# Optimization experiments

Hardware: AMD Instinct MI355X
Metric: run time of the kernel (lower is better)

Reference implementation:

```python
import jax, jax.numpy as jnp
import numpy as np

B, S, D, H = 2, 1024, 1024, 16
DH = D // H
EPS = 1e-5

def _ln(x, g, b):
    m = jnp.mean(x, axis=-1, keepdims=True)
    v = jnp.mean((x - m) ** 2, axis=-1, keepdims=True)
    return (x - m) / jnp.sqrt(v + EPS) * g + b

def setup_inputs() -> dict:
    key = jax.random.key(0)
    ks = jax.random.split(key, 5)
    scale = 1.0 / np.sqrt(D)
    return {
        "id": jax.random.normal(ks[0], (B, S, D), dtype=jnp.float32),
        "Wq": jax.random.uniform(ks[1], (D, D), jnp.float32, -scale, scale),
        "Wk": jax.random.uniform(ks[2], (D, D), jnp.float32, -scale, scale),
        "Wv": jax.random.uniform(ks[3], (D, D), jnp.float32, -scale, scale),
        "g0": jnp.ones((D,), jnp.float32), "b0": jnp.zeros((D,), jnp.float32),
        "g1": jnp.ones((D,), jnp.float32), "b1": jnp.zeros((D,), jnp.float32),
        "g2": jnp.ones((D,), jnp.float32), "b2": jnp.zeros((D,), jnp.float32),
    }

def reference(id, Wq, Wk, Wv, g0, b0, g1, b1, g2, b2):
    residual = id
    id_ln = _ln(id, g0, b0)
    # torch Linear: x @ W.T ; split heads along last dim, cat along batch
    q = (id_ln @ Wq.T).reshape(B, S, H, DH)
    k = (id_ln @ Wk.T).reshape(B, S, H, DH)
    v = (id_ln @ Wv.T).reshape(B, S, H, DH)
    scores = jnp.einsum('bqhd,bkhd->bhqk', q, k) / np.sqrt(DH)
    A = jax.nn.softmax(scores, axis=-1)                      # [B,H,S,S]
    O = jnp.einsum('bhqk,bkhd->bqhd', A, v).reshape(B, S, D)  # merge heads
    left = _ln(id_ln + O, g1, b1)
    right = _ln(residual + O, g2, b2)
    out = left + right
    # torch layout of A is [(H*B), S, S] with head-major ordering
    A_out = jnp.transpose(A, (1, 0, 2, 3)).reshape(H * B, S, S)
    return (out, A_out)
```

## Files before the change

kernel.cpp:

```cpp
#include <hip/hip_runtime.h>

namespace {

constexpr int B = 2, S = 1024, D = 1024, H = 16, DH = 64;
constexpr int M = B * S;
constexpr float EPS = 1e-5f;

using bf16x8 = __attribute__((ext_vector_type(8))) short;
using f32x4  = __attribute__((ext_vector_type(4))) float;

typedef const __attribute__((address_space(1))) void* gptr_t;
typedef __attribute__((address_space(3))) void* lptr_t;

__device__ __forceinline__ unsigned short f2bf(float f) {
    union { float f; unsigned u; } v{f};
    unsigned r = v.u + 0x7fffu + ((v.u >> 16) & 1u);
    return (unsigned short)(r >> 16);
}

__device__ __forceinline__ float wave_sum(float v) {
#pragma unroll
    for (int off = 32; off > 0; off >>= 1) v += __shfl_down(v, off, 64);
    return v;
}

__global__ __launch_bounds__(256) void cvt_w_kernel(
    const float* __restrict__ Wq, const float* __restrict__ Wk,
    const float* __restrict__ Wv, unsigned short* __restrict__ Wb)
{
    const float* src = (blockIdx.z == 0) ? Wq : (blockIdx.z == 1) ? Wk : Wv;
    const size_t i = ((size_t)blockIdx.x * 256 + threadIdx.x) * 4;
    float4 f = *reinterpret_cast<const float4*>(src + i);
    ushort4 h;
    h.x = f2bf(f.x); h.y = f2bf(f.y); h.z = f2bf(f.z); h.w = f2bf(f.w);
    *reinterpret_cast<ushort4*>(Wb + (size_t)blockIdx.z * D * D + i) = h;
}

__global__ __launch_bounds__(256) void ln0_kernel(
    const float* __restrict__ x, const float* __restrict__ g,
    const float* __restrict__ bt, float* __restrict__ y,
    unsigned short* __restrict__ yb)
{
    __shared__ float sm[8];
    __shared__ float stats[2];
    const int row = blockIdx.x;
    const int t = threadIdx.x;
    const float4 v = reinterpret_cast<const float4*>(x + (size_t)row * D)[t];
    float s  = v.x + v.y + v.z + v.w;
    float ss = v.x*v.x + v.y*v.y + v.z*v.z + v.w*v.w;
    s = wave_sum(s); ss = wave_sum(ss);
    const int lane = t & 63, wid = t >> 6;
    if (lane == 0) { sm[wid] = s; sm[4 + wid] = ss; }
    __syncthreads();
    if (t == 0) {
        float S1 = sm[0] + sm[1] + sm[2] + sm[3];
        float S2 = sm[4] + sm[5] + sm[6] + sm[7];
        float m  = S1 * (1.0f / D);
        float var = S2 * (1.0f / D) - m * m;
        stats[0] = m; stats[1] = rsqrtf(var + EPS);
    }
    __syncthreads();
    const float m = stats[0], r = stats[1];
    const float4 gv = reinterpret_cast<const float4*>(g)[t];
    const float4 bv = reinterpret_cast<const float4*>(bt)[t];
    float4 o;
    o.x = (v.x - m) * r * gv.x + bv.x;
    o.y = (v.y - m) * r * gv.y + bv.y;
    o.z = (v.z - m) * r * gv.z + bv.z;
    o.w = (v.w - m) * r * gv.w + bv.w;
    reinterpret_cast<float4*>(y + (size_t)row * D)[t] = o;
    ushort4 h; h.x = f2bf(o.x); h.y = f2bf(o.y); h.z = f2bf(o.z); h.w = f2bf(o.w);
    *reinterpret_cast<ushort4*>(yb + (size_t)row * D + t * 4) = h;
}

__global__ __launch_bounds__(256) void qkv_mfma_kernel(
    const unsigned short* __restrict__ idln, const unsigned short* __restrict__ Wb,
    unsigned short* __restrict__ q, unsigned short* __restrict__ k,
    unsigned short* __restrict__ vT)
{
    __shared__ unsigned short As[128 * 32];
    __shared__ unsigned short Bs[128 * 32];
    const int zi = blockIdx.z;
    const unsigned short* Bmat = Wb + (size_t)zi * D * D;
    const int m0 = blockIdx.y * 128, n0 = blockIdx.x * 128;
    const int t = threadIdx.x;
    const int w = t >> 6, lane = t & 63;
    const int wm = (w >> 1) * 64, wn = (w & 1) * 64;
    const int quad = lane >> 4, l16 = lane & 15;
    const int srow = t >> 2;
    const int scol = (t & 3) * 8;

    f32x4 acc[4][4];
#pragma unroll
    for (int i = 0; i < 4; ++i)
#pragma unroll
        for (int j = 0; j < 4; ++j) acc[i][j] = (f32x4){0.f, 0.f, 0.f, 0.f};

    for (int k0 = 0; k0 < D; k0 += 32) {
        __syncthreads();
#pragma unroll
        for (int c = 0; c < 2; ++c) {
            const unsigned short* ga = idln + (size_t)(m0 + srow + c * 64) * D + k0 + scol;
            __builtin_amdgcn_global_load_lds((gptr_t)ga, (lptr_t)(As + t * 8 + c * 2048), 16, 0, 0);
            const unsigned short* gb = Bmat + (size_t)(n0 + srow + c * 64) * D + k0 + scol;
            __builtin_amdgcn_global_load_lds((gptr_t)gb, (lptr_t)(Bs + t * 8 + c * 2048), 16, 0, 0);
        }
        __syncthreads();
        bf16x8 af[4], bfr[4];
#pragma unroll
        for (int i = 0; i < 4; ++i)
            af[i] = *reinterpret_cast<const bf16x8*>(As + (wm + i * 16 + l16) * 32 + quad * 8);
#pragma unroll
        for (int j = 0; j < 4; ++j)
            bfr[j] = *reinterpret_cast<const bf16x8*>(Bs + (wn + j * 16 + l16) * 32 + quad * 8);
#pragma unroll
        for (int i = 0; i < 4; ++i)
#pragma unroll
            for (int j = 0; j < 4; ++j)
                acc[i][j] = __builtin_amdgcn_mfma_f32_16x16x32_bf16(af[i], bfr[j], acc[i][j], 0, 0, 0);
    }

    if (zi < 2) {
        unsigned short* C = (zi == 0) ? q : k;
#pragma unroll
        for (int i = 0; i < 4; ++i)
#pragma unroll
            for (int j = 0; j < 4; ++j) {
                const int gcol = n0 + wn + j * 16 + l16;
#pragma unroll
                for (int reg = 0; reg < 4; ++reg) {
                    const int grow = m0 + wm + i * 16 + quad * 4 + reg;
                    C[(size_t)grow * D + gcol] = f2bf(acc[i][j][reg]);
                }
            }
    } else {
        const int b = m0 >> 10;
#pragma unroll
        for (int i = 0; i < 4; ++i)
#pragma unroll
            for (int j = 0; j < 4; ++j) {
                const int gcol = n0 + wn + j * 16 + l16;
                const int srow0 = (m0 - b * S) + wm + i * 16 + quad * 4;
                ushort4 h;
                h.x = f2bf(acc[i][j][0]); h.y = f2bf(acc[i][j][1]);
                h.z = f2bf(acc[i][j][2]); h.w = f2bf(acc[i][j][3]);
                *reinterpret_cast<ushort4*>(vT + ((size_t)b * D + gcol) * S + srow0) = h;
            }
    }
}

__global__ __launch_bounds__(256) void scores_mfma_kernel(
    const unsigned short* __restrict__ q, const unsigned short* __restrict__ k,
    float* __restrict__ Eout, float* __restrict__ rowsum)
{
    __shared__ unsigned short As[128 * 32];
    __shared__ unsigned short Bs[128 * 32];
    const int z = blockIdx.z;
    const int b = z & 1, h = z >> 1;
    const int m0 = blockIdx.y * 128, n0 = blockIdx.x * 128;
    const int t = threadIdx.x;
    const int w = t >> 6, lane = t & 63;
    const int wm = (w >> 1) * 64, wn = (w & 1) * 64;
    const int quad = lane >> 4, l16 = lane & 15;
    const int srow = t >> 2;
    const int scol = (t & 3) * 8;

    f32x4 acc[4][4];
#pragma unroll
    for (int i = 0; i < 4; ++i)
#pragma unroll
        for (int j = 0; j < 4; ++j) acc[i][j] = (f32x4){0.f, 0.f, 0.f, 0.f};

    for (int k0 = 0; k0 < DH; k0 += 32) {
        __syncthreads();
#pragma unroll
        for (int c = 0; c < 2; ++c) {
            const unsigned short* ga = q + (size_t)(b * S + m0 + srow + c * 64) * D + h * DH + k0 + scol;
            __builtin_amdgcn_global_load_lds((gptr_t)ga, (lptr_t)(As + t * 8 + c * 2048), 16, 0, 0);
            const unsigned short* gb = k + (size_t)(b * S + n0 + srow + c * 64) * D + h * DH + k0 + scol;
            __builtin_amdgcn_global_load_lds((gptr_t)gb, (lptr_t)(Bs + t * 8 + c * 2048), 16, 0, 0);
        }
        __syncthreads();
        bf16x8 af[4], bfr[4];
#pragma unroll
        for (int i = 0; i < 4; ++i)
            af[i] = *reinterpret_cast<const bf16x8*>(As + (wm + i * 16 + l16) * 32 + quad * 8);
#pragma unroll
        for (int j = 0; j < 4; ++j)
            bfr[j] = *reinterpret_cast<const bf16x8*>(Bs + (wn + j * 16 + l16) * 32 + quad * 8);
#pragma unroll
        for (int i = 0; i < 4; ++i)
#pragma unroll
            for (int j = 0; j < 4; ++j)
                acc[i][j] = __builtin_amdgcn_mfma_f32_16x16x32_bf16(af[i], bfr[j], acc[i][j], 0, 0, 0);
    }

    float* Ez = Eout + (size_t)z * S * S;
    float part[4][4];
#pragma unroll
    for (int i = 0; i < 4; ++i)
#pragma unroll
        for (int reg = 0; reg < 4; ++reg) part[i][reg] = 0.f;

#pragma unroll
    for (int i = 0; i < 4; ++i)
#pragma unroll
        for (int j = 0; j < 4; ++j) {
            const int gcol = n0 + wn + j * 16 + l16;
#pragma unroll
            for (int reg = 0; reg < 4; ++reg) {
                const int grow = m0 + wm + i * 16 + quad * 4 + reg;
                float e = __expf(acc[i][j][reg] * 0.125f);
                Ez[(size_t)grow * S + gcol] = e;
                part[i][reg] += e;
            }
        }
#pragma unroll
    for (int i = 0; i < 4; ++i)
#pragma unroll
        for (int reg = 0; reg < 4; ++reg) {
            float p = part[i][reg];
#pragma unroll
            for (int off = 1; off < 16; off <<= 1) p += __shfl_xor(p, off, 64);
            part[i][reg] = p;
        }
    if (l16 == 0) {
#pragma unroll
        for (int i = 0; i < 4; ++i)
#pragma unroll
            for (int reg = 0; reg < 4; ++reg) {
                const int grow = m0 + wm + i * 16 + quad * 4 + reg;
                atomicAdd(&rowsum[(size_t)z * S + grow], part[i][reg]);
            }
    }
}

__global__ __launch_bounds__(256) void ov_mfma_kernel(
    float* __restrict__ Eio, const unsigned short* __restrict__ vT,
    const float* __restrict__ rowsum, float* __restrict__ O)
{
    __shared__ unsigned short Es[128 * 32];
    __shared__ unsigned short Vs[64 * 32];
    __shared__ float sInv[128];
    const int z = blockIdx.z;
    const int b = z & 1, h = z >> 1;
    const int m0 = blockIdx.y * 128;
    const int t = threadIdx.x;
    const int w = t >> 6, lane = t & 63;
    const int wm = w * 32;
    const int quad = lane >> 4, l16 = lane & 15;

    if (t < 128) sInv[t] = 1.0f / rowsum[(size_t)z * S + m0 + t];

    float* Ez = Eio + (size_t)z * S * S;

    f32x4 acc[2][4];
#pragma unroll
    for (int i = 0; i < 2; ++i)
#pragma unroll
        for (int j = 0; j < 4; ++j) acc[i][j] = (f32x4){0.f, 0.f, 0.f, 0.f};

    const int er = t >> 1;
    const int ec = (t & 1) * 16;

    for (int k0 = 0; k0 < S; k0 += 32) {
        __syncthreads();
        {
            const unsigned short* gv = vT + ((size_t)b * D + h * DH + (t >> 2)) * S + k0 + (t & 3) * 8;
            __builtin_amdgcn_global_load_lds((gptr_t)gv, (lptr_t)(Vs + t * 8), 16, 0, 0);
        }
        {
            float* gE = Ez + (size_t)(m0 + er) * S + k0 + ec;
            const float inv = sInv[er];
#pragma unroll
            for (int u = 0; u < 4; ++u) {
                float4 f = *reinterpret_cast<const float4*>(gE + u * 4);
                float4 fn = make_float4(f.x * inv, f.y * inv, f.z * inv, f.w * inv);
                *reinterpret_cast<float4*>(gE + u * 4) = fn;
                ushort4 hh;
                hh.x = f2bf(f.x); hh.y = f2bf(f.y); hh.z = f2bf(f.z); hh.w = f2bf(f.w);
                *reinterpret_cast<ushort4*>(Es + er * 32 + ec + u * 4) = hh;
            }
        }
        __syncthreads();
        bf16x8 af[2], bfr[4];
#pragma unroll
        for (int i = 0; i < 2; ++i)
            af[i] = *reinterpret_cast<const bf16x8*>(Es + (wm + i * 16 + l16) * 32 + quad * 8);
#pragma unroll
        for (int j = 0; j < 4; ++j)
            bfr[j] = *reinterpret_cast<const bf16x8*>(Vs + (j * 16 + l16) * 32 + quad * 8);
#pragma unroll
        for (int i = 0; i < 2; ++i)
#pragma unroll
            for (int j = 0; j < 4; ++j)
                acc[i][j] = __builtin_amdgcn_mfma_f32_16x16x32_bf16(af[i], bfr[j], acc[i][j], 0, 0, 0);
    }

#pragma unroll
    for (int i = 0; i < 2; ++i)
#pragma unroll
        for (int j = 0; j < 4; ++j) {
            const int gcol = h * DH + j * 16 + l16;
#pragma unroll
            for (int reg = 0; reg < 4; ++reg) {
                const int lrow = wm + i * 16 + quad * 4 + reg;
                O[(size_t)(b * S + m0 + lrow) * D + gcol] = acc[i][j][reg] * sInv[lrow];
            }
        }
}

__global__ __launch_bounds__(256) void final_kernel(
    const float* __restrict__ id, const float* __restrict__ id_ln, const float* __restrict__ O,
    const float* __restrict__ g1, const float* __restrict__ b1,
    const float* __restrict__ g2, const float* __restrict__ b2,
    float* __restrict__ out)
{
    __shared__ float sm[16];
    __shared__ float stats[4];
    const int row = blockIdx.x;
    const int t = threadIdx.x;
    const size_t base = (size_t)row * D;
    const float4 xi = reinterpret_cast<const float4*>(id + base)[t];
    const float4 xl = reinterpret_cast<const float4*>(id_ln + base)[t];
    const float4 xo = reinterpret_cast<const float4*>(O + base)[t];
    float4 t1, t2;
    t1.x = xl.x + xo.x; t1.y = xl.y + xo.y; t1.z = xl.z + xo.z; t1.w = xl.w + xo.w;
    t2.x = xi.x + xo.x; t2.y = xi.y + xo.y; t2.z = xi.z + xo.z; t2.w = xi.w + xo.w;
    float s1  = t1.x + t1.y + t1.z + t1.w;
    float ss1 = t1.x*t1.x + t1.y*t1.y + t1.z*t1.z + t1.w*t1.w;
    float s2  = t2.x + t2.y + t2.z + t2.w;
    float ss2 = t2.x*t2.x + t2.y*t2.y + t2.z*t2.z + t2.w*t2.w;
    s1 = wave_sum(s1); ss1 = wave_sum(ss1);
    s2 = wave_sum(s2); ss2 = wave_sum(ss2);
    const int lane = t & 63, wid = t >> 6;
    if (lane == 0) { sm[wid] = s1; sm[4+wid] = ss1; sm[8+wid] = s2; sm[12+wid] = ss2; }
    __syncthreads();
    if (t == 0) {
        float S1 = sm[0]+sm[1]+sm[2]+sm[3];
        float Q1 = sm[4]+sm[5]+sm[6]+sm[7];
        float S2 = sm[8]+sm[9]+sm[10]+sm[11];
        float Q2 = sm[12]+sm[13]+sm[14]+sm[15];
        float m1 = S1 * (1.0f / D);
        float m2 = S2 * (1.0f / D);
        stats[0] = m1; stats[1] = rsqrtf(Q1 * (1.0f / D) - m1*m1 + EPS);
        stats[2] = m2; stats[3] = rsqrtf(Q2 * (1.0f / D) - m2*m2 + EPS);
    }
    __syncthreads();
    const float m1 = stats[0], r1 = stats[1], m2 = stats[2], r2 = stats[3];
    const float4 g1v = reinterpret_cast<const float4*>(g1)[t];
    const float4 b1v = reinterpret_cast<const float4*>(b1)[t];
    const float4 g2v = reinterpret_cast<const float4*>(g2)[t];
    const float4 b2v = reinterpret_cast<const float4*>(b2)[t];
    float4 o;
    o.x = (t1.x - m1)*r1*g1v.x + b1v.x + (t2.x - m2)*r2*g2v.x + b2v.x;
    o.y = (t1.y - m1)*r1*g1v.y + b1v.y + (t2.y - m2)*r2*g2v.y + b2v.y;
    o.z = (t1.z - m1)*r1*g1v.z + b1v.z + (t2.z - m2)*r2*g2v.z + b2v.z;
    o.w = (t1.w - m1)*r1*g1v.w + b1v.w + (t2.w - m2)*r2*g2v.w + b2v.w;
    reinterpret_cast<float4*>(out + base)[t] = o;
}

}

extern "C" void kernel_launch(void* const* d_in, const int* in_sizes, int n_in,
                              void* d_out, int out_size, void* d_ws, size_t ws_size,
                              hipStream_t stream)
{
    const float* id = (const float*)d_in[0];
    const float* Wq = (const float*)d_in[1];
    const float* Wk = (const float*)d_in[2];
    const float* Wv = (const float*)d_in[3];
    const float* g0 = (const float*)d_in[4];
    const float* b0 = (const float*)d_in[5];
    const float* g1 = (const float*)d_in[6];
    const float* b1 = (const float*)d_in[7];
    const float* g2 = (const float*)d_in[8];
    const float* b2 = (const float*)d_in[9];

    float* out  = (float*)d_out;
    float* Eout = out + (size_t)B * S * D;

    char* ws = (char*)d_ws;
    float* id_ln  = (float*)(ws);
    float* O      = (float*)(ws + (8u << 20));
    float* rowsum = (float*)(ws + (16u << 20));
    unsigned short* idln_bf = (unsigned short*)(ws + (16u << 20) + (128u << 10));
    unsigned short* Wb      = idln_bf + (size_t)M * D;
    unsigned short* qb      = Wb + (size_t)3 * D * D;
    unsigned short* kb      = qb + (size_t)M * D;
    unsigned short* vT      = kb + (size_t)M * D;

    hipMemsetAsync(rowsum, 0, (size_t)H * B * S * sizeof(float), stream);
    hipLaunchKernelGGL(cvt_w_kernel, dim3(D * D / 1024, 1, 3), dim3(256), 0, stream,
                       Wq, Wk, Wv, Wb);
    hipLaunchKernelGGL(ln0_kernel, dim3(M), dim3(256), 0, stream, id, g0, b0, id_ln, idln_bf);
    hipLaunchKernelGGL(qkv_mfma_kernel, dim3(D / 128, M / 128, 3), dim3(256), 0, stream,
                       idln_bf, Wb, qb, kb, vT);
    hipLaunchKernelGGL(scores_mfma_kernel, dim3(S / 128, S / 128, H * B), dim3(256), 0, stream,
                       qb, kb, Eout, rowsum);
    hipLaunchKernelGGL(ov_mfma_kernel, dim3(1, S / 128, H * B), dim3(256), 0, stream,
                       Eout, vT, rowsum, O);
    hipLaunchKernelGGL(final_kernel, dim3(M), dim3(256), 0, stream,
                       id, id_ln, O, g1, b1, g2, b2, out);
}
```

Baseline: 276.1 us.

## Fuse scores and PV into one two-pass attention kernel

Replaces the separate scores kernel (writing unnormalized exp to A, plus atomic row sums) and the PV kernel (re-reading A, normalizing, writing back) with one kernel per 64-row query tile. The first pass computes QK^T only to accumulate row sums. The second pass recomputes QK^T, writes normalized A once, and feeds bf16 probabilities from LDS into the PV MFMA. This removes a full read and rewrite of the 128 MB attention matrix, the memset and the atomics. The cost is doubled QK^T compute and more LDS per block.

After: 233.3 us. -15.5%, faster.

```diff
diff --git a/kernel.cpp b/kernel.cpp
--- a/kernel.cpp
+++ b/kernel.cpp
@@ -149,164 +149,157 @@
     }
 }
 
-__global__ __launch_bounds__(256) void scores_mfma_kernel(
+__global__ __launch_bounds__(256) void attn_fused_kernel(
     const unsigned short* __restrict__ q, const unsigned short* __restrict__ k,
-    float* __restrict__ Eout, float* __restrict__ rowsum)
-{
-    __shared__ unsigned short As[128 * 32];
-    __shared__ unsigned short Bs[128 * 32];
+    const unsigned short* __restrict__ vT, float* __restrict__ Aout,
+    float* __restrict__ O)
+{
+    __shared__ unsigned short Qs[2 * 64 * 32];
+    __shared__ unsigned short Ks[2 * 128 * 32];
+    __shared__ unsigned short Vs[4 * 64 * 32];
+    __shared__ unsigned short Ps[4 * 64 * 32];
+    __shared__ float rs[4][64];
+    __shared__ float sInv[64];
+
     const int z = blockIdx.z;
     const int b = z & 1, h = z >> 1;
-    const int m0 = blockIdx.y * 128, n0 = blockIdx.x * 128;
+    const int m0 = blockIdx.y * 64;
     const int t = threadIdx.x;
     const int w = t >> 6, lane = t & 63;
-    const int wm = (w >> 1) * 64, wn = (w & 1) * 64;
     const int quad = lane >> 4, l16 = lane & 15;
-    const int srow = t >> 2;
-    const int scol = (t & 3) * 8;
-
-    f32x4 acc[4][4];
+    const int wn = w * 32;
+    const int sr = t >> 2, sc8 = (t & 3) * 8;
+
+#pragma unroll
+    for (int c = 0; c < 2; ++c) {
+        const unsigned short* gq = q + (size_t)(b * S + m0 + sr) * D + h * DH + c * 32 + sc8;
+        __builtin_amdgcn_global_load_lds((gptr_t)gq, (lptr_t)(Qs + c * 2048 + t * 8), 16, 0, 0);
+    }
+
+    float part[4][4];
 #pragma unroll
     for (int i = 0; i < 4; ++i)
 #pragma unroll
-        for (int j = 0; j < 4; ++j) acc[i][j] = (f32x4){0.f, 0.f, 0.f, 0.f};
-
-    for (int k0 = 0; k0 < DH; k0 += 32) {
-        __syncthreads();
+        for (int r = 0; r < 4; ++r) part[i][r] = 0.f;
+
+    for (int n0 = 0; n0 < S; n0 += 128) {
+        __syncthreads();
+#pragma unroll
+        for (int c = 0; c < 2; ++c)
+#pragma unroll
+            for (int cc = 0; cc < 2; ++cc) {
+                const unsigned short* gk = k + (size_t)(b * S + n0 + cc * 64 + sr) * D + h * DH + c * 32 + sc8;
+                __builtin_amdgcn_global_load_lds((gptr_t)gk, (lptr_t)(Ks + c * 4096 + cc * 2048 + t * 8), 16, 0, 0);
+            }
+        __syncthreads();
+        f32x4 acc[4][2];
+#pragma unroll
+        for (int i = 0; i < 4; ++i)
+#pragma unroll
+            for (int j = 0; j < 2; ++j) acc[i][j] = (f32x4){0.f, 0.f, 0.f, 0.f};
 #pragma unroll
         for (int c = 0; c < 2; ++c) {
-            const unsigned short* ga = q + (size_t)(b * S + m0 + srow + c * 64) * D + h * DH + k0 + scol;
-            __builtin_amdgcn_global_load_lds((gptr_t)ga, (lptr_t)(As + t * 8 + c * 2048), 16, 0, 0);
-            const unsigned short* gb = k + (size_t)(b * S + n0 + srow + c * 64) * D + h * DH + k0 + scol;
-            __builtin_amdgcn_global_load_lds((gptr_t)gb, (lptr_t)(Bs + t * 8 + c * 2048), 16, 0, 0);
-        }
-        __syncthreads();
-        bf16x8 af[4], bfr[4];
-#pragma unroll
-        for (int i = 0; i < 4; ++i)
-            af[i] = *reinterpret_cast<const bf16x8*>(As + (wm + i * 16 + l16) * 32 + quad * 8);
-#pragma unroll
-        for (int j = 0; j < 4; ++j)
-            bfr[j] = *reinterpret_cast<const bf16x8*>(Bs + (wn + j * 16 + l16) * 32 + quad * 8);
-#pragma unroll
-        for (int i = 0; i < 4; ++i)
-#pragma unroll
-            for (int j = 0; j < 4; ++j)
-                acc[i][j] = __builtin_amdgcn_mfma_f32_16x16x32_bf16(af[i], bfr[j], acc[i][j], 0, 0, 0);
-    }
-
-    float* Ez = Eout + (size_t)z * S * S;
-    float part[4][4];
+            bf16x8 af[4], bfr[2];
+#pragma unroll
+            for (int i = 0; i < 4; ++i)
+                af[i] = *reinterpret_cast<const bf16x8*>(Qs + c * 2048 + (i * 16 + l16) * 32 + quad * 8);
+#pragma unroll
+            for (int j = 0; j < 2; ++j)
+                bfr[j] = *reinterpret_cast<const bf16x8*>(Ks + c * 4096 + (wn + j * 16 + l16) * 32 + quad * 8);
+#pragma unroll
+            for (int i = 0; i < 4; ++i)
+#pragma unroll
+                for (int j = 0; j < 2; ++j)
+                    acc[i][j] = __builtin_amdgcn_mfma_f32_16x16x32_bf16(af[i], bfr[j], acc[i][j], 0, 0, 0);
+        }
+#pragma unroll
+        for (int i = 0; i < 4; ++i)
+#pragma unroll
+            for (int j = 0; j < 2; ++j)
+#pragma unroll
+                for (int r = 0; r < 4; ++r)
+                    part[i][r] += __expf(acc[i][j][r] * 0.125f);
+    }
 #pragma unroll
     for (int i = 0; i < 4; ++i)
 #pragma unroll
-        for (int reg = 0; reg < 4; ++reg) part[i][reg] = 0.f;
-
-#pragma unroll
-    for (int i = 0; i < 4; ++i)
-#pragma unroll
-        for (int j = 0; j < 4; ++j) {
-            const int gcol = n0 + wn + j * 16 + l16;
-#pragma unroll
-            for (int reg = 0; reg < 4; ++reg) {
-                const int grow = m0 + wm + i * 16 + quad * 4 + reg;
-                float e = __expf(acc[i][j][reg] * 0.125f);
-                Ez[(size_t)grow * S + gcol] = e;
-                part[i][reg] += e;
-            }
-        }
-#pragma unroll
-    for (int i = 0; i < 4; ++i)
-#pragma unroll
-        for (int reg = 0; reg < 4; ++reg) {
-            float p = part[i][reg];
+        for (int r = 0; r < 4; ++r) {
+            float p = part[i][r];
 #pragma unroll
             for (int off = 1; off < 16; off <<= 1) p += __shfl_xor(p, off, 64);
-            part[i][reg] = p;
-        }
-    if (l16 == 0) {
-#pragma unroll
-        for (int i = 0; i < 4; ++i)
-#pragma unroll
-            for (int reg = 0; reg < 4; ++reg) {
-                const int grow = m0 + wm + i * 16 + quad * 4 + reg;
-                atomicAdd(&rowsum[(size_t)z * S + grow], part[i][reg]);
-            }
-    }
-}
-
-__global__ __launch_bounds__(256) void ov_mfma_kernel(
-    float* __restrict__ Eio, const unsigned short* __restrict__ vT,
-    const float* __restrict__ rowsum, float* __restrict__ O)
-{
-    __shared__ unsigned short Es[128 * 32];
-    __shared__ unsigned short Vs[64 * 32];
-    __shared__ float sInv[128];
-    const int z = blockIdx.z;
-    const int b = z & 1, h = z >> 1;
-    const int m0 = blockIdx.y * 128;
-    const int t = threadIdx.x;
-    const int w = t >> 6, lane = t & 63;
-    const int wm = w * 32;
-    const int quad = lane >> 4, l16 = lane & 15;
-
-    if (t < 128) sInv[t] = 1.0f / rowsum[(size_t)z * S + m0 + t];
-
-    float* Ez = Eio + (size_t)z * S * S;
-
-    f32x4 acc[2][4];
-#pragma unroll
-    for (int i = 0; i < 2; ++i)
-#pragma unroll
-        for (int j = 0; j < 4; ++j) acc[i][j] = (f32x4){0.f, 0.f, 0.f, 0.f};
-
-    const int er = t >> 1;
-    const int ec = (t & 1) * 16;
-
-    for (int k0 = 0; k0 < S; k0 += 32) {
-        __syncthreads();
-        {
-            const unsigned short* gv = vT + ((size_t)b * D + h * DH + (t >> 2)) * S + k0 + (t & 3) * 8;
-            __builtin_amdgcn_global_load_lds((gptr_t)gv, (lptr_t)(Vs + t * 8), 16, 0, 0);
-        }
-        {
-            float* gE = Ez + (size_t)(m0 + er) * S + k0 + ec;
-            const float inv = sInv[er];
-#pragma unroll
-            for (int u = 0; u < 4; ++u) {
-                float4 f = *reinterpret_cast<const float4*>(gE + u * 4);
-                float4 fn = make_float4(f.x * inv, f.y * inv, f.z * inv, f.w * inv);
-                *reinterpret_cast<float4*>(gE + u * 4) = fn;
-                ushort4 hh;
-                hh.x = f2bf(f.x); hh.y = f2bf(f.y); hh.z = f2bf(f.z); hh.w = f2bf(f.w);
-                *reinterpret_cast<ushort4*>(Es + er * 32 + ec + u * 4) = hh;
-            }
-        }
-        __syncthreads();
-        bf16x8 af[2], bfr[4];
-#pragma unroll
-        for (int i = 0; i < 2; ++i)
-            af[i] = *reinterpret_cast<const bf16x8*>(Es + (wm + i * 16 + l16) * 32 + quad * 8);
-#pragma unroll
-        for (int j = 0; j < 4; ++j)
-            bfr[j] = *reinterpret_cast<const bf16x8*>(Vs + (j * 16 + l16) * 32 + quad * 8);
-#pragma unroll
-        for (int i = 0; i < 2; ++i)
-#pragma unroll
-            for (int j = 0; j < 4; ++j)
-                acc[i][j] = __builtin_amdgcn_mfma_f32_16x16x32_bf16(af[i], bfr[j], acc[i][j], 0, 0, 0);
-    }
-
-#pragma unroll
-    for (int i = 0; i < 2; ++i)
-#pragma unroll
-        for (int j = 0; j < 4; ++j) {
-            const int gcol = h * DH + j * 16 + l16;
-#pragma unroll
-            for (int reg = 0; reg < 4; ++reg) {
-                const int lrow = wm + i * 16 + quad * 4 + reg;
-                O[(size_t)(b * S + m0 + lrow) * D + gcol] = acc[i][j][reg] * sInv[lrow];
-            }
+            if (l16 == 0) rs[w][i * 16 + quad * 4 + r] = p;
+        }
+    __syncthreads();
+    if (t < 64) sInv[t] = 1.0f / (rs[0][t] + rs[1][t] + rs[2][t] + rs[3][t]);
+
+    float* Az = Aout + (size_t)z * S * S;
+    f32x4 accO[4];
+#pragma unroll
+    for (int j = 0; j < 4; ++j) accO[j] = (f32x4){0.f, 0.f, 0.f, 0.f};
+
+    for (int n0 = 0; n0 < S; n0 += 128) {
+        __syncthreads();
+#pragma unroll
+        for (int c = 0; c < 2; ++c)
+#pragma unroll
+            for (int cc = 0; cc < 2; ++cc) {
+                const unsigned short* gk = k + (size_t)(b * S + n0 + cc * 64 + sr) * D + h * DH + c * 32 + sc8;
+                __builtin_amdgcn_global_load_lds((gptr_t)gk, (lptr_t)(Ks + c * 4096 + cc * 2048 + t * 8), 16, 0, 0);
+            }
+#pragma unroll
+        for (int ks = 0; ks < 4; ++ks) {
+            const unsigned short* gv = vT + ((size_t)b * D + h * DH + sr) * S + n0 + ks * 32 + sc8;
+            __builtin_amdgcn_global_load_lds((gptr_t)gv, (lptr_t)(Vs + ks * 2048 + t * 8), 16, 0, 0);
+        }
+        __syncthreads();
+        f32x4 acc[4][2];
+#pragma unroll
+        for (int i = 0; i < 4; ++i)
+#pragma unroll
+            for (int j = 0; j < 2; ++j) acc[i][j] = (f32x4){0.f, 0.f, 0.f, 0.f};
+#pragma unroll
+        for (int c = 0; c < 2; ++c) {
+            bf16x8 af[4], bfr[2];
+#pragma unroll
+            for (int i = 0; i < 4; ++i)
+                af[i] = *reinterpret_cast<const bf16x8*>(Qs + c * 2048 + (i * 16 + l16) * 32 + quad * 8);
+#pragma unroll
+            for (int j = 0; j < 2; ++j)
+                bfr[j] = *reinterpret_cast<const bf16x8*>(Ks + c * 4096 + (wn + j * 16 + l16) * 32 + quad * 8);
+#pragma unroll
+            for (int i = 0; i < 4; ++i)
+#pragma unroll
+                for (int j = 0; j < 2; ++j)
+                    acc[i][j] = __builtin_amdgcn_mfma_f32_16x16x32_bf16(af[i], bfr[j], acc[i][j], 0, 0, 0);
+        }
+#pragma unroll
+        for (int i = 0; i < 4; ++i)
+#pragma unroll
+            for (int j = 0; j < 2; ++j)
+#pragma unroll
+                for (int r = 0; r < 4; ++r) {
+                    const int rl = i * 16 + quad * 4 + r;
+                    float a = __expf(acc[i][j][r] * 0.125f) * sInv[rl];
+                    Az[(size_t)(m0 + rl) * S + n0 + wn + j * 16 + l16] = a;
+                    Ps[w * 2048 + rl * 32 + j * 16 + l16] = f2bf(a);
+                }
+        __syncthreads();
+#pragma unroll
+        for (int ks = 0; ks < 4; ++ks) {
+            bf16x8 af = *reinterpret_cast<const bf16x8*>(Ps + ks * 2048 + (w * 16 + l16) * 32 + quad * 8);
+#pragma unroll
+            for (int j = 0; j < 4; ++j) {
+                bf16x8 bfr = *reinterpret_cast<const bf16x8*>(Vs + ks * 2048 + (j * 16 + l16) * 32 + quad * 8);
+                accO[j] = __builtin_amdgcn_mfma_f32_16x16x32_bf16(af, bfr, accO[j], 0, 0, 0);
+            }
+        }
+    }
+#pragma unroll
+    for (int j = 0; j < 4; ++j)
+#pragma unroll
+        for (int r = 0; r < 4; ++r) {
+            const int grow = b * S + m0 + w * 16 + quad * 4 + r;
+            O[(size_t)grow * D + h * DH + j * 16 + l16] = accO[j][r];
         }
 }
 
@@ -378,28 +371,24 @@
     const float* b2 = (const float*)d_in[9];
 
     float* out  = (float*)d_out;
-    float* Eout = out + (size_t)B * S * D;
+    float* Aout = out + (size_t)B * S * D;
 
     char* ws = (char*)d_ws;
     float* id_ln  = (float*)(ws);
     float* O      = (float*)(ws + (8u << 20));
-    float* rowsum = (float*)(ws + (16u << 20));
-    unsigned short* idln_bf = (unsigned short*)(ws + (16u << 20) + (128u << 10));
+    unsigned short* idln_bf = (unsigned short*)(ws + (16u << 20));
     unsigned short* Wb      = idln_bf + (size_t)M * D;
     unsigned short* qb      = Wb + (size_t)3 * D * D;
     unsigned short* kb      = qb + (size_t)M * D;
     unsigned short* vT      = kb + (size_t)M * D;
 
-    hipMemsetAsync(rowsum, 0, (size_t)H * B * S * sizeof(float), stream);
     hipLaunchKernelGGL(cvt_w_kernel, dim3(D * D / 1024, 1, 3), dim3(256), 0, stream,
                        Wq, Wk, Wv, Wb);
     hipLaunchKernelGGL(ln0_kernel, dim3(M), dim3(256), 0, stream, id, g0, b0, id_ln, idln_bf);
     hipLaunchKernelGGL(qkv_mfma_kernel, dim3(D / 128, M / 128, 3), dim3(256), 0, stream,
                        idln_bf, Wb, qb, kb, vT);
-    hipLaunchKernelGGL(scores_mfma_kernel, dim3(S / 128, S / 128, H * B), dim3(256), 0, stream,
-                       qb, kb, Eout, rowsum);
-    hipLaunchKernelGGL(ov_mfma_kernel, dim3(1, S / 128, H * B), dim3(256), 0, stream,
-                       Eout, vT, rowsum, O);
+    hipLaunchKernelGGL(attn_fused_kernel, dim3(1, S / 64, H * B), dim3(256), 0, stream,
+                       qb, kb, vT, Aout, O);
     hipLaunchKernelGGL(final_kernel, dim3(M), dim3(256), 0, stream,
                        id, id_ln, O, g1, b1, g2, b2, out);
 }
```
